# Performance work log

Hardware: AMD Instinct MI355X
Metric: run time of the kernel (lower is better)

The kernel has to match this reference:

```python
import jax, jax.numpy as jnp
import numpy as np

NB_CLASSES = 100000
SZ_EMBED = 64
SZ_BATCH = 1024


def setup_inputs() -> dict:
    key = jax.random.key(0)
    k1, k2, k3 = jax.random.split(key, 3)
    xs = jax.random.normal(k1, (SZ_BATCH, SZ_EMBED), dtype=jnp.float32)
    ys = jax.random.randint(k2, (SZ_BATCH,), 0, NB_CLASSES, dtype=jnp.int64)
    # xavier_uniform for an Embedding(nb_classes, sz_embed)
    limit = float(np.sqrt(6.0 / (NB_CLASSES + SZ_EMBED)))
    proxies = jax.random.uniform(k3, (NB_CLASSES, SZ_EMBED), dtype=jnp.float32,
                                 minval=-limit, maxval=limit)
    return {"xs": xs, "ys": ys, "proxies": proxies}


def reference(xs, ys, proxies):
    # L2-normalize each proxy row (torch F.normalize; eps guard like torch's 1e-12).
    # Note: the original normalizes the positive proxy with dim=0 on a 1-D vector,
    # which is identical to per-row normalization.
    norms = jnp.linalg.norm(proxies, axis=1, keepdims=True)
    P = proxies / jnp.maximum(norms, 1e-12)                      # [C, D]

    # Squared euclidean distance matrix D[i, c] = ||x_i - P_c||^2 via GEMM
    x_sq = jnp.sum(xs * xs, axis=1, keepdims=True)               # [B, 1]
    p_sq = jnp.sum(P * P, axis=1)                                # [C]
    dist = jnp.maximum(x_sq + p_sq[None, :] - 2.0 * (xs @ P.T), 0.0)  # [B, C]

    logits = -dist                                               # [B, C]
    ys = ys.astype(jnp.int32)
    d_pos = jnp.take_along_axis(dist, ys[:, None], axis=1)[:, 0]  # [B]

    # log sum over negatives (c != y) of exp(-dist)
    neg_mask = jnp.arange(NB_CLASSES)[None, :] != ys[:, None]    # [B, C]
    neg_logits = jnp.where(neg_mask, logits, -jnp.inf)
    log_n = jax.nn.logsumexp(neg_logits, axis=1)                 # [B]

    # -log(p / n) = dist_pos + log(sum_neg exp(-dist))
    per_sample = d_pos + log_n
    return jnp.mean(per_sample)
```

## Files before the change

kernel.cpp:

```cpp
#include <hip/hip_runtime.h>
#include <math.h>

#define B 1024
#define C 100000
#define D 64
#define MT 128
#define TC 256
#define NCH 391
#define NPADROWS (NCH * TC)
#define CPAD (NPADROWS - C)
#define PPR (NCH * 4)
#define L2E 1.4426950408889634f

typedef __attribute__((ext_vector_type(8))) short short8;
typedef __attribute__((ext_vector_type(4))) float f32x4;

#define WS_PART 0
#define WS_CW2  ((size_t)B * PPR * 4)
#define WS_XBF  (WS_CW2 + B * 4)
#define WS_PBF  (WS_XBF + (size_t)B * D * 2)

#define GLB(p) ((const __attribute__((address_space(1))) void*)(p))
#define LDS(p) ((__attribute__((address_space(3))) void*)(p))

static __device__ __forceinline__ unsigned short f2bf(float f) {
    unsigned u = __float_as_uint(f);
    return (unsigned short)((u + 0x7fffu + ((u >> 16) & 1u)) >> 16);
}
static __device__ __forceinline__ float bf_round(float f) {
    return __uint_as_float(((unsigned)f2bf(f)) << 16);
}
static __device__ __forceinline__ float fexp2(float x) {
#if __has_builtin(__builtin_amdgcn_exp2f)
    return __builtin_amdgcn_exp2f(x);
#else
    return __expf(x * 0.6931471805599453f);
#endif
}

__global__ __launch_bounds__(256) void proxynca_prep(
    const float* __restrict__ xs, const float* __restrict__ proxies,
    unsigned short* __restrict__ Xbf, unsigned short* __restrict__ Pbf,
    float* __restrict__ cw2)
{
    const int t = threadIdx.x;
    const int rl = t >> 4, f4 = t & 15;
    const int bb = blockIdx.x;
    if (bb < NPADROWS / 16) {
        int gr = bb * 16 + rl;
        float4 v = make_float4(0.f, 0.f, 0.f, 0.f);
        if (gr < C) v = *(const float4*)(proxies + (size_t)gr * D + f4 * 4);
        float ss = v.x*v.x + v.y*v.y + v.z*v.z + v.w*v.w;
        ss += __shfl_xor(ss, 1); ss += __shfl_xor(ss, 2);
        ss += __shfl_xor(ss, 4); ss += __shfl_xor(ss, 8);
        float rn = 1.0f / fmaxf(sqrtf(ss), 1e-12f);
        ushort4 w;
        w.x = f2bf(v.x * rn); w.y = f2bf(v.y * rn);
        w.z = f2bf(v.z * rn); w.w = f2bf(v.w * rn);
        *(ushort4*)(Pbf + (size_t)gr * D + f4 * 4) = w;
    } else {
        int row = (bb - NPADROWS / 16) * 16 + rl;
        float4 v = *(const float4*)(xs + (size_t)row * D + f4 * 4);
        float ss = v.x*v.x + v.y*v.y + v.z*v.z + v.w*v.w;
        ss += __shfl_xor(ss, 1); ss += __shfl_xor(ss, 2);
        ss += __shfl_xor(ss, 4); ss += __shfl_xor(ss, 8);
        ushort4 w;
        w.x = f2bf(v.x); w.y = f2bf(v.y); w.z = f2bf(v.z); w.w = f2bf(v.w);
        *(ushort4*)(Xbf + (size_t)row * D + f4 * 4) = w;
        if (f4 == 0) cw2[row] = -2.0f * sqrtf(ss) * L2E;
    }
}

__global__ __launch_bounds__(512, 4) void proxynca_main(
    const unsigned short* __restrict__ Xbf, const unsigned short* __restrict__ Pbf,
    const float* __restrict__ cw2v, float* __restrict__ partial)
{
    __shared__ __align__(16) unsigned short Ash[MT * 64];
    __shared__ __align__(16) unsigned short Bsh[TC * 64];
    __shared__ float crow[MT];

    const int t = threadIdx.x;
    const int lane = t & 63;
    const int wv = t >> 6;
    const int row0 = blockIdx.x * MT;
    const int ct = blockIdx.y;

    const unsigned short* Asrc = Xbf + (size_t)row0 * D;
    const unsigned short* Bsrc = Pbf + (size_t)ct * TC * D;

    #pragma unroll
    for (int j = 0; j < 2; ++j) {
        int c = (j * 8 + wv) * 64 + lane;
        int row = c >> 3, q = c & 7;
        int sc = (row << 3) | (q ^ (row & 7));
        __builtin_amdgcn_global_load_lds(GLB(Asrc + sc * 8),
            LDS(Ash + (size_t)(j * 8 + wv) * 512), 16, 0, 0);
    }
    #pragma unroll
    for (int j = 0; j < 4; ++j) {
        int c = (j * 8 + wv) * 64 + lane;
        int row = c >> 3, q = c & 7;
        int sc = (row << 3) | (q ^ (row & 7));
        __builtin_amdgcn_global_load_lds(GLB(Bsrc + sc * 8),
            LDS(Bsh + (size_t)(j * 8 + wv) * 512), 16, 0, 0);
    }
    if (t < MT) crow[t] = cw2v[row0 + t];
    __syncthreads();

    const int quad = lane >> 4, sixt = lane & 15;
    const int mg = wv >> 2, ng = wv & 3;

    short8 af[4][2];
    #pragma unroll
    for (int ms = 0; ms < 4; ++ms) {
        int rowL = mg * 64 + ms * 16 + sixt;
        int sw = rowL & 7;
        af[ms][0] = *(const short8*)(Ash + (size_t)(((rowL << 3) | (quad ^ sw)) * 8));
        af[ms][1] = *(const short8*)(Ash + (size_t)(((rowL << 3) | ((4 + quad) ^ sw)) * 8));
    }
    float cw[4][4];
    #pragma unroll
    for (int ms = 0; ms < 4; ++ms)
        #pragma unroll
        for (int rg = 0; rg < 4; ++rg)
            cw[ms][rg] = crow[mg * 64 + ms * 16 + quad * 4 + rg];

    float s_acc[4][4];
    #pragma unroll
    for (int ms = 0; ms < 4; ++ms)
        #pragma unroll
        for (int rg = 0; rg < 4; ++rg) s_acc[ms][rg] = 0.f;

    #pragma unroll
    for (int ns = 0; ns < 4; ++ns) {
        int classL = ng * 64 + ns * 16 + sixt;
        int sw = classL & 7;
        short8 b0 = *(const short8*)(Bsh + (size_t)(((classL << 3) | (quad ^ sw)) * 8));
        short8 b1 = *(const short8*)(Bsh + (size_t)(((classL << 3) | ((4 + quad) ^ sw)) * 8));
        #pragma unroll
        for (int ms = 0; ms < 4; ++ms) {
            f32x4 acc = {0.f, 0.f, 0.f, 0.f};
            acc = __builtin_amdgcn_mfma_f32_16x16x32_bf16(af[ms][0], b0, acc, 0, 0, 0);
            acc = __builtin_amdgcn_mfma_f32_16x16x32_bf16(af[ms][1], b1, acc, 0, 0, 0);
            #pragma unroll
            for (int rg = 0; rg < 4; ++rg)
                s_acc[ms][rg] += fexp2(fmaf(2.0f * L2E, acc[rg], cw[ms][rg]));
        }
    }

    #pragma unroll
    for (int ms = 0; ms < 4; ++ms)
        #pragma unroll
        for (int rg = 0; rg < 4; ++rg) {
            float s = s_acc[ms][rg];
            s += __shfl_xor(s, 1); s += __shfl_xor(s, 2);
            s += __shfl_xor(s, 4); s += __shfl_xor(s, 8);
            s_acc[ms][rg] = s;
        }
    if (sixt == 0) {
        #pragma unroll
        for (int ms = 0; ms < 4; ++ms)
            #pragma unroll
            for (int rg = 0; rg < 4; ++rg) {
                int row = row0 + mg * 64 + ms * 16 + quad * 4 + rg;
                partial[(size_t)row * PPR + ct * 4 + ng] = s_acc[ms][rg];
            }
    }
}

__global__ __launch_bounds__(256) void proxynca_reduce(
    const float* __restrict__ xs, const int* __restrict__ ys,
    const float* __restrict__ proxies, const float* __restrict__ partial,
    float* __restrict__ out)
{
    __shared__ float acc4[4];
    const int lane = threadIdx.x & 63;
    const int w = threadIdx.x >> 6;
    const int row = blockIdx.x * 4 + w;

    float x = xs[(size_t)row * D + lane];
    int y = ys[row];
    float p = proxies[(size_t)y * D + lane];

    float xx = x * x, pp = p * p;
    #pragma unroll
    for (int off = 1; off < 64; off <<= 1) {
        xx += __shfl_xor(xx, off);
        pp += __shfl_xor(pp, off);
    }
    float nx = sqrtf(xx);
    float rn = 1.0f / fmaxf(sqrtf(pp), 1e-12f);
    float ph = p * rn;

    float xp = x * ph;
    float xpb = bf_round(x) * bf_round(ph);
    #pragma unroll
    for (int off = 1; off < 64; off <<= 1) {
        xp  += __shfl_xor(xp, off);
        xpb += __shfl_xor(xpb, off);
    }

    float s = 0.f;
    for (int j = lane; j < PPR; j += 64) s += partial[(size_t)row * PPR + j];
    #pragma unroll
    for (int off = 1; off < 64; off <<= 1) s += __shfl_xor(s, off);

    if (lane == 0) {
        float cw2r = -2.0f * nx * L2E;
        float e_pos = fexp2(fmaf(2.0f * L2E, xpb, cw2r));
        float e_pad = fexp2(cw2r);
        float s_neg = s - e_pos - (float)CPAD * e_pad;
        acc4[w] = 2.0f * (nx - xp) + logf(s_neg);
    }
    __syncthreads();
    if (threadIdx.x == 0) {
        float v = acc4[0] + acc4[1] + acc4[2] + acc4[3];
        atomicAdd(out, v * (1.0f / (float)B));
    }
}

extern "C" void kernel_launch(void* const* d_in, const int* in_sizes, int n_in,
                              void* d_out, int out_size, void* d_ws, size_t ws_size,
                              hipStream_t stream)
{
    const float* xs      = (const float*)d_in[0];
    const int*   ys      = (const int*)d_in[1];
    const float* proxies = (const float*)d_in[2];
    char* ws = (char*)d_ws;
    float* partial = (float*)(ws + WS_PART);
    float* cw2     = (float*)(ws + WS_CW2);
    unsigned short* Xbf = (unsigned short*)(ws + WS_XBF);
    unsigned short* Pbf = (unsigned short*)(ws + WS_PBF);
    float* out = (float*)d_out;

    hipMemsetAsync(out, 0, sizeof(float), stream);
    proxynca_prep<<<NPADROWS / 16 + B / 16, 256, 0, stream>>>(xs, proxies, Xbf, Pbf, cw2);
    dim3 gridA(B / MT, NCH);
    proxynca_main<<<gridA, 512, 0, stream>>>(Xbf, Pbf, cw2, partial);
    proxynca_reduce<<<B / 4, 256, 0, stream>>>(xs, ys, proxies, partial, out);
}
```

Baseline: 121.5 us.

## Fold exp scale into X, bias into MFMA accumulator, DPP transpose-reduce

Pre-scales X by 2*log2(e) during bf16 conversion and seeds the MFMA accumulator with the per-row bias. This removes the per-element FMA before exp2 and the shared-memory staging of the bias row. The 16-lane row-sum epilogue is replaced by a DPP-based transpose reduction, so every lane writes one partial instead of shuffling all 16 values and having one lane in 16 write. The scaling changes bf16 rounding slightly, and the reduce kernel is updated to match.

```diff
diff --git a/kernel.cpp b/kernel.cpp
--- a/kernel.cpp
+++ b/kernel.cpp
@@ -11,6 +11,7 @@
 #define CPAD (NPADROWS - C)
 #define PPR (NCH * 4)
 #define L2E 1.4426950408889634f
+#define SCL2 (2.0f * L2E)
 
 typedef __attribute__((ext_vector_type(8))) short short8;
 typedef __attribute__((ext_vector_type(4))) float f32x4;
@@ -37,6 +38,9 @@
     return __expf(x * 0.6931471805599453f);
 #endif
 }
+
+#define DPPF(x, ctrl) __uint_as_float((unsigned)__builtin_amdgcn_update_dpp( \
+    0, (int)__float_as_uint(x), (ctrl), 0xF, 0xF, true))
 
 __global__ __launch_bounds__(256) void proxynca_prep(
     const float* __restrict__ xs, const float* __restrict__ proxies,
@@ -65,7 +69,8 @@
         ss += __shfl_xor(ss, 1); ss += __shfl_xor(ss, 2);
         ss += __shfl_xor(ss, 4); ss += __shfl_xor(ss, 8);
         ushort4 w;
-        w.x = f2bf(v.x); w.y = f2bf(v.y); w.z = f2bf(v.z); w.w = f2bf(v.w);
+        w.x = f2bf(v.x * SCL2); w.y = f2bf(v.y * SCL2);
+        w.z = f2bf(v.z * SCL2); w.w = f2bf(v.w * SCL2);
         *(ushort4*)(Xbf + (size_t)row * D + f4 * 4) = w;
         if (f4 == 0) cw2[row] = -2.0f * sqrtf(ss) * L2E;
     }
@@ -77,7 +82,6 @@
 {
     __shared__ __align__(16) unsigned short Ash[MT * 64];
     __shared__ __align__(16) unsigned short Bsh[TC * 64];
-    __shared__ float crow[MT];
 
     const int t = threadIdx.x;
     const int lane = t & 63;
@@ -104,11 +108,16 @@
         __builtin_amdgcn_global_load_lds(GLB(Bsrc + sc * 8),
             LDS(Bsh + (size_t)(j * 8 + wv) * 512), 16, 0, 0);
     }
-    if (t < MT) crow[t] = cw2v[row0 + t];
-    __syncthreads();
 
     const int quad = lane >> 4, sixt = lane & 15;
     const int mg = wv >> 2, ng = wv & 3;
+
+    f32x4 cwv[4];
+    #pragma unroll
+    for (int ms = 0; ms < 4; ++ms)
+        cwv[ms] = *(const f32x4*)(cw2v + row0 + mg * 64 + ms * 16 + quad * 4);
+
+    __syncthreads();
 
     short8 af[4][2];
     #pragma unroll
@@ -118,18 +127,10 @@
         af[ms][0] = *(const short8*)(Ash + (size_t)(((rowL << 3) | (quad ^ sw)) * 8));
         af[ms][1] = *(const short8*)(Ash + (size_t)(((rowL << 3) | ((4 + quad) ^ sw)) * 8));
     }
-    float cw[4][4];
-    #pragma unroll
-    for (int ms = 0; ms < 4; ++ms)
-        #pragma unroll
-        for (int rg = 0; rg < 4; ++rg)
-            cw[ms][rg] = crow[mg * 64 + ms * 16 + quad * 4 + rg];
-
-    float s_acc[4][4];
-    #pragma unroll
-    for (int ms = 0; ms < 4; ++ms)
-        #pragma unroll
-        for (int rg = 0; rg < 4; ++rg) s_acc[ms][rg] = 0.f;
+
+    f32x4 s_vec[4];
+    #pragma unroll
+    for (int ms = 0; ms < 4; ++ms) s_vec[ms] = (f32x4){0.f, 0.f, 0.f, 0.f};
 
     #pragma unroll
     for (int ns = 0; ns < 4; ++ns) {
@@ -139,33 +140,54 @@
         short8 b1 = *(const short8*)(Bsh + (size_t)(((classL << 3) | ((4 + quad) ^ sw)) * 8));
         #pragma unroll
         for (int ms = 0; ms < 4; ++ms) {
-            f32x4 acc = {0.f, 0.f, 0.f, 0.f};
-            acc = __builtin_amdgcn_mfma_f32_16x16x32_bf16(af[ms][0], b0, acc, 0, 0, 0);
+            f32x4 acc = __builtin_amdgcn_mfma_f32_16x16x32_bf16(af[ms][0], b0, cwv[ms], 0, 0, 0);
             acc = __builtin_amdgcn_mfma_f32_16x16x32_bf16(af[ms][1], b1, acc, 0, 0, 0);
+            f32x4 e;
             #pragma unroll
-            for (int rg = 0; rg < 4; ++rg)
-                s_acc[ms][rg] += fexp2(fmaf(2.0f * L2E, acc[rg], cw[ms][rg]));
-        }
-    }
-
+            for (int rg = 0; rg < 4; ++rg) e[rg] = fexp2(acc[rg]);
+            s_vec[ms] += e;
+        }
+    }
+
+    float v[16];
     #pragma unroll
     for (int ms = 0; ms < 4; ++ms)
         #pragma unroll
-        for (int rg = 0; rg < 4; ++rg) {
-            float s = s_acc[ms][rg];
-            s += __shfl_xor(s, 1); s += __shfl_xor(s, 2);
-            s += __shfl_xor(s, 4); s += __shfl_xor(s, 8);
-            s_acc[ms][rg] = s;
-        }
-    if (sixt == 0) {
-        #pragma unroll
-        for (int ms = 0; ms < 4; ++ms)
-            #pragma unroll
-            for (int rg = 0; rg < 4; ++rg) {
-                int row = row0 + mg * 64 + ms * 16 + quad * 4 + rg;
-                partial[(size_t)row * PPR + ct * 4 + ng] = s_acc[ms][rg];
-            }
-    }
+        for (int rg = 0; rg < 4; ++rg) v[ms * 4 + rg] = s_vec[ms][rg];
+
+    {   bool b = (sixt & 8) != 0;
+        #pragma unroll
+        for (int j = 0; j < 8; ++j) {
+            float k = b ? v[j + 8] : v[j];
+            float s = b ? v[j] : v[j + 8];
+            v[j] = k + DPPF(s, 0x140);
+        }
+    }
+    {   bool b = (sixt & 4) != 0;
+        #pragma unroll
+        for (int j = 0; j < 4; ++j) {
+            float k = b ? v[j + 4] : v[j];
+            float s = b ? v[j] : v[j + 4];
+            v[j] = k + DPPF(s, 0x141);
+        }
+    }
+    {   bool b = (sixt & 2) != 0;
+        #pragma unroll
+        for (int j = 0; j < 2; ++j) {
+            float k = b ? v[j + 2] : v[j];
+            float s = b ? v[j] : v[j + 2];
+            v[j] = k + DPPF(s, 0x4E);
+        }
+    }
+    {   bool b = (sixt & 1) != 0;
+        float k = b ? v[1] : v[0];
+        float s = b ? v[0] : v[1];
+        v[0] = k + DPPF(s, 0xB1);
+    }
+
+    int msf = sixt >> 2, rgf = sixt & 3;
+    int row = row0 + mg * 64 + msf * 16 + quad * 4 + rgf;
+    partial[(size_t)row * PPR + ct * 4 + ng] = v[0];
 }
 
 __global__ __launch_bounds__(256) void proxynca_reduce(
@@ -193,7 +215,7 @@
     float ph = p * rn;
 
     float xp = x * ph;
-    float xpb = bf_round(x) * bf_round(ph);
+    float xpb = bf_round(x * SCL2) * bf_round(ph);
     #pragma unroll
     for (int off = 1; off < 64; off <<= 1) {
         xp  += __shfl_xor(xp, off);
@@ -207,7 +229,7 @@
 
     if (lane == 0) {
         float cw2r = -2.0f * nx * L2E;
-        float e_pos = fexp2(fmaf(2.0f * L2E, xpb, cw2r));
+        float e_pos = fexp2(xpb + cw2r);
         float e_pad = fexp2(cw2r);
         float s_neg = s - e_pos - (float)CPAD * e_pad;
         acc4[w] = 2.0f * (nx - xp) + logf(s_neg);
```

Result: faster. 115.4 us (-5.1%).
